# Optimization experiments

Measured on AMD Instinct MI355X. Metric: run time of the kernel, lower is better.

The kernel has to match this reference:

```python
import jax, jax.numpy as jnp
import numpy as np

N_NODES = 100000
N_EDGES = 1600000
IN_FEATS = 256
HEADS = 4
OUT_FEATS = 32


def setup_inputs() -> dict:
    key = jax.random.key(0)
    k1, k2, k3, k4, k5, k6 = jax.random.split(key, 6)
    feat = jax.random.normal(k1, (N_NODES, IN_FEATS), dtype=jnp.float32)
    fc_w = jax.random.normal(k2, (HEADS * OUT_FEATS, IN_FEATS), dtype=jnp.float32) * (1.0 / np.sqrt(IN_FEATS))
    attn_l = jax.random.normal(k3, (1, HEADS, OUT_FEATS), dtype=jnp.float32) * 0.1
    attn_r = jax.random.normal(k4, (1, HEADS, OUT_FEATS), dtype=jnp.float32) * 0.1
    src = jax.random.randint(k5, (N_EDGES,), 0, N_NODES, dtype=jnp.int32)
    dst = jax.random.randint(k6, (N_EDGES,), 0, N_NODES, dtype=jnp.int32)
    return {"feat": feat, "fc_w": fc_w, "attn_l": attn_l, "attn_r": attn_r, "src": src, "dst": dst}


def reference(feat, fc_w, attn_l, attn_r, src, dst):
    # feat: [N, F_in]; fc_w: [H*D, F_in]; attn_l/r: [1, H, D]; src/dst: [E]
    N = feat.shape[0]
    H, D = attn_l.shape[1], attn_l.shape[2]
    # linear projection (no bias), viewed as [N, H, D]
    ft = (feat @ fc_w.T).reshape(N, H, D)
    # per-node attention logits
    el = jnp.einsum('nhd,hd->nh', ft, attn_l[0])  # [N, H]
    er = jnp.einsum('nhd,hd->nh', ft, attn_r[0])  # [N, H]
    # per-edge score: leaky_relu(el[src] + er[dst])
    e = jax.nn.leaky_relu(el[src] + er[dst], negative_slope=0.2)  # [E, H]
    # edge softmax over incoming edges of each dst node (stable)
    emax = jax.ops.segment_max(e, dst, num_segments=N)  # [N, H]
    a = jnp.exp(e - emax[dst])  # [E, H]
    asum = jax.ops.segment_sum(a, dst, num_segments=N)  # [N, H]
    a = a / asum[dst]
    # attn_drop is a no-op in eval mode; weighted scatter-sum aggregation
    msg = ft[src] * a[:, :, None]  # [E, H, D]
    out = jax.ops.segment_sum(msg, dst, num_segments=N)  # [N, H, D]
    # final_layer=False, activation=None, norm=None -> flatten heads
    return out.reshape(N, H * D)
```

## Files before the change

kernel.cpp:

```cpp
#include <hip/hip_runtime.h>
#include <hip/hip_bf16.h>
#include <float.h>

#define IN_F 256
#define HD   128
#define NH   4
#define GM   128

typedef __bf16 bf16x8 __attribute__((ext_vector_type(8)));
typedef __bf16 bf16x2 __attribute__((ext_vector_type(2)));
typedef float  f32x4  __attribute__((ext_vector_type(4)));

__device__ __forceinline__ bf16x8 cvt8(const float4 a, const float4 b) {
    bf16x8 r;
    r[0] = (__bf16)a.x; r[1] = (__bf16)a.y; r[2] = (__bf16)a.z; r[3] = (__bf16)a.w;
    r[4] = (__bf16)b.x; r[5] = (__bf16)b.y; r[6] = (__bf16)b.z; r[7] = (__bf16)b.w;
    return r;
}

__global__ __launch_bounds__(256) void gemm_fused(const float* __restrict__ feat,
                                                  const float* __restrict__ w,
                                                  const float* __restrict__ attn_l,
                                                  const float* __restrict__ attn_r,
                                                  const int* __restrict__ dst,
                                                  __bf16* __restrict__ ft,
                                                  float* __restrict__ el,
                                                  float* __restrict__ er,
                                                  int* __restrict__ deg,
                                                  int* __restrict__ rank,
                                                  int N, int E, int ntiles) {
    __shared__ __align__(16) __bf16 Bs[128][264];
    __shared__ __align__(16) __bf16 As[GM][40];
    const int t = threadIdx.x;
    const int wv = t >> 6;
    const int lane = t & 63;

    {
        const int col = t >> 1;
        const int koff = (t & 1) * 128;
        const float* wp = w + (size_t)col * IN_F + koff;
#pragma unroll
        for (int i = 0; i < 128; i += 8) {
            const float4 v0 = *(const float4*)(wp + i);
            const float4 v1 = *(const float4*)(wp + i + 4);
            *(bf16x8*)&Bs[col][koff + i] = cvt8(v0, v1);
        }
    }

    for (int i = blockIdx.x * 256 + t; i < E; i += gridDim.x * 256)
        rank[i] = atomicAdd(&deg[dst[i]], 1);

    const int frow = lane & 15;
    const int fk   = (lane >> 4) * 8;

    float alw[8], arw[8];
#pragma unroll
    for (int ct = 0; ct < 8; ++ct) {
        alw[ct] = attn_l[ct * 16 + frow];
        arw[ct] = attn_r[ct * 16 + frow];
    }

    const int ar_ = t >> 1;
    const int ac  = (t & 1) * 16;

    float4 p0, p1, p2, p3;
    {
        const int gr = blockIdx.x * GM + ar_;
        if (gr < N) {
            const float* fp = feat + (size_t)gr * IN_F + ac;
            p0 = *(const float4*)(fp);
            p1 = *(const float4*)(fp + 4);
            p2 = *(const float4*)(fp + 8);
            p3 = *(const float4*)(fp + 12);
        } else {
            p0 = p1 = p2 = p3 = make_float4(0.f, 0.f, 0.f, 0.f);
        }
    }

    for (int tile = blockIdx.x; tile < ntiles; tile += gridDim.x) {
        const int row0 = tile * GM;
        f32x4 acc[2][8];
#pragma unroll
        for (int mt = 0; mt < 2; ++mt)
#pragma unroll
            for (int ct = 0; ct < 8; ++ct) acc[mt][ct] = {0.f, 0.f, 0.f, 0.f};

        for (int ks = 0; ks < 8; ++ks) {
            __syncthreads();
            *(bf16x8*)&As[ar_][ac]     = cvt8(p0, p1);
            *(bf16x8*)&As[ar_][ac + 8] = cvt8(p2, p3);

            const int ntile = (ks < 7) ? tile : tile + gridDim.x;
            const int nks   = (ks < 7) ? ks + 1 : 0;
            if (ntile < ntiles) {
                const int gr = ntile * GM + ar_;
                if (gr < N) {
                    const float* fp = feat + (size_t)gr * IN_F + nks * 32 + ac;
                    p0 = *(const float4*)(fp);
                    p1 = *(const float4*)(fp + 4);
                    p2 = *(const float4*)(fp + 8);
                    p3 = *(const float4*)(fp + 12);
                } else {
                    p0 = p1 = p2 = p3 = make_float4(0.f, 0.f, 0.f, 0.f);
                }
            }

            __syncthreads();
            const int k0 = ks * 32;
            const bf16x8 af0 = *(const bf16x8*)&As[wv * 32 + frow][fk];
            const bf16x8 af1 = *(const bf16x8*)&As[wv * 32 + 16 + frow][fk];
#pragma unroll
            for (int ct = 0; ct < 8; ++ct) {
                const bf16x8 bfrag = *(const bf16x8*)&Bs[ct * 16 + frow][k0 + fk];
                acc[0][ct] = __builtin_amdgcn_mfma_f32_16x16x32_bf16(af0, bfrag, acc[0][ct], 0, 0, 0);
                acc[1][ct] = __builtin_amdgcn_mfma_f32_16x16x32_bf16(af1, bfrag, acc[1][ct], 0, 0, 0);
            }
        }

        const int rb = row0 + wv * 32 + (lane >> 4) * 4;
        if (row0 + GM <= N) {
#pragma unroll
            for (int mt = 0; mt < 2; ++mt)
#pragma unroll
                for (int ct = 0; ct < 8; ++ct)
#pragma unroll
                    for (int reg = 0; reg < 4; ++reg) {
                        const int m = rb + mt * 16 + reg;
                        ft[(size_t)m * HD + ct * 16 + frow] = (__bf16)acc[mt][ct][reg];
                    }
        } else {
#pragma unroll
            for (int mt = 0; mt < 2; ++mt)
#pragma unroll
                for (int ct = 0; ct < 8; ++ct)
#pragma unroll
                    for (int reg = 0; reg < 4; ++reg) {
                        const int m = rb + mt * 16 + reg;
                        if (m < N) ft[(size_t)m * HD + ct * 16 + frow] = (__bf16)acc[mt][ct][reg];
                    }
        }

#pragma unroll
        for (int mt = 0; mt < 2; ++mt) {
#pragma unroll
            for (int reg = 0; reg < 4; ++reg) {
                float pl[4], pr[4];
#pragma unroll
                for (int h = 0; h < 4; ++h) {
                    const float v0 = acc[mt][2 * h][reg];
                    const float v1 = acc[mt][2 * h + 1][reg];
                    pl[h] = v0 * alw[2 * h] + v1 * alw[2 * h + 1];
                    pr[h] = v0 * arw[2 * h] + v1 * arw[2 * h + 1];
                }
#pragma unroll
                for (int s = 1; s < 16; s <<= 1) {
#pragma unroll
                    for (int h = 0; h < 4; ++h) {
                        pl[h] += __shfl_xor(pl[h], s);
                        pr[h] += __shfl_xor(pr[h], s);
                    }
                }
                if (frow == 0) {
                    const int r = row0 + wv * 32 + mt * 16 + (lane >> 4) * 4 + reg;
                    if (r < N) {
                        *(float4*)(el + (size_t)r * NH) = make_float4(pl[0], pl[1], pl[2], pl[3]);
                        *(float4*)(er + (size_t)r * NH) = make_float4(pr[0], pr[1], pr[2], pr[3]);
                    }
                }
            }
        }
    }
}

__global__ __launch_bounds__(1024) void scan1_k(const int* __restrict__ deg,
                                                int* __restrict__ off,
                                                int* __restrict__ bsum, int N) {
    __shared__ int lds[1024];
    const int t = threadIdx.x;
    const int g = blockIdx.x * 1024 + t;
    const int x = (g < N) ? deg[g] : 0;
    lds[t] = x;
    __syncthreads();
    int v = x;
    for (int s = 1; s < 1024; s <<= 1) {
        const int add = (t >= s) ? lds[t - s] : 0;
        __syncthreads();
        v += add;
        lds[t] = v;
        __syncthreads();
    }
    if (g < N) off[g] = v - x;
    if (t == 1023) bsum[blockIdx.x] = v;
}

__global__ __launch_bounds__(128) void scan2_k(const int* __restrict__ bsum,
                                               int* __restrict__ boff, int nb) {
    __shared__ int lds[128];
    const int t = threadIdx.x;
    const int x = (t < nb) ? bsum[t] : 0;
    lds[t] = x;
    __syncthreads();
    int v = x;
    for (int s = 1; s < 128; s <<= 1) {
        const int add = (t >= s) ? lds[t - s] : 0;
        __syncthreads();
        v += add;
        lds[t] = v;
        __syncthreads();
    }
    boff[t] = v - x;
}

__global__ __launch_bounds__(256) void scatter_k(const int* __restrict__ src,
                                                 const int* __restrict__ dst,
                                                 const int* __restrict__ off,
                                                 const int* __restrict__ boff,
                                                 const int* __restrict__ rank,
                                                 int* __restrict__ ssrc, int E) {
    const int i = blockIdx.x * 256 + threadIdx.x;
    if (i < E) {
        const int d = dst[i];
        const int p = off[d] + boff[d >> 10] + rank[i];
        ssrc[p] = src[i];
    }
}

__global__ __launch_bounds__(64) void aggregate_k(const __bf16* __restrict__ ft,
                                                  const float* __restrict__ el,
                                                  const float* __restrict__ er,
                                                  const int* __restrict__ deg,
                                                  const int* __restrict__ off,
                                                  const int* __restrict__ boff,
                                                  const int* __restrict__ ssrc,
                                                  float* __restrict__ out, int N) {
    const int n = blockIdx.x;
    const int lane = threadIdx.x;
    const int il = lane & 15;
    const int q  = lane >> 4;
    const int h  = il >> 2;
    float4* outp = (float4*)(out + (size_t)n * HD);
    const int dn = deg[n];
    if (dn == 0) {
        if (q < 2) outp[il * 2 + q] = make_float4(0.f, 0.f, 0.f, 0.f);
        return;
    }
    const int start = off[n] + boff[n >> 10];
    const float4 er4 = *(const float4*)(er + (size_t)n * NH);

    __shared__ float a_lds[64 * NH];
    __shared__ int   s_lds[64];
    float4 ssum = make_float4(0.f, 0.f, 0.f, 0.f);
    float acc[8];
#pragma unroll
    for (int i = 0; i < 8; ++i) acc[i] = 0.f;

    for (int c0 = 0; c0 < dn; c0 += 64) {
        const int j = c0 + lane;
        float4 a = make_float4(0.f, 0.f, 0.f, 0.f);
        int sv = 0;
        if (j < dn) {
            sv = ssrc[start + j];
            float4 e = *(const float4*)(el + (size_t)sv * NH);
            e.x += er4.x; e.y += er4.y; e.z += er4.z; e.w += er4.w;
            e.x = e.x >= 0.f ? e.x : 0.2f * e.x;
            e.y = e.y >= 0.f ? e.y : 0.2f * e.y;
            e.z = e.z >= 0.f ? e.z : 0.2f * e.z;
            e.w = e.w >= 0.f ? e.w : 0.2f * e.w;
            a.x = __expf(e.x); a.y = __expf(e.y);
            a.z = __expf(e.z); a.w = __expf(e.w);
            ssum.x += a.x; ssum.y += a.y; ssum.z += a.z; ssum.w += a.w;
        }
        s_lds[lane] = sv;
        *(float4*)(a_lds + lane * NH) = a;
        __syncthreads();
        const int cnt = min(64, dn - c0);
        for (int j2 = 0; j2 < cnt; j2 += 8) {
            const int e0 = j2 + q;
            const int e1 = j2 + 4 + q;
            const int sv0 = s_lds[e0];
            const int sv1 = s_lds[e1];
            const float a0 = a_lds[e0 * NH + h];
            const float a1 = a_lds[e1 * NH + h];
            const bf16x8 f0 = *(const bf16x8*)(ft + (size_t)sv0 * HD + il * 8);
            const bf16x8 f1 = *(const bf16x8*)(ft + (size_t)sv1 * HD + il * 8);
#pragma unroll
            for (int k = 0; k < 8; ++k) acc[k] = fmaf(a0, (float)f0[k], acc[k]);
#pragma unroll
            for (int k = 0; k < 8; ++k) acc[k] = fmaf(a1, (float)f1[k], acc[k]);
        }
        __syncthreads();
    }
#pragma unroll
    for (int s = 1; s < 64; s <<= 1) {
        ssum.x += __shfl_xor(ssum.x, s);
        ssum.y += __shfl_xor(ssum.y, s);
        ssum.z += __shfl_xor(ssum.z, s);
        ssum.w += __shfl_xor(ssum.w, s);
    }
#pragma unroll
    for (int k = 0; k < 8; ++k) {
        acc[k] += __shfl_xor(acc[k], 16);
        acc[k] += __shfl_xor(acc[k], 32);
    }
    const float sumh = (h == 0) ? ssum.x : (h == 1) ? ssum.y : (h == 2) ? ssum.z : ssum.w;
    const float inv = 1.f / sumh;
    if (q < 2) {
        const int b = q * 4;
        outp[il * 2 + q] = make_float4(acc[b] * inv, acc[b + 1] * inv,
                                       acc[b + 2] * inv, acc[b + 3] * inv);
    }
}

extern "C" void kernel_launch(void* const* d_in, const int* in_sizes, int n_in,
                              void* d_out, int out_size, void* d_ws, size_t ws_size,
                              hipStream_t stream) {
    const float* feat   = (const float*)d_in[0];
    const float* fc_w   = (const float*)d_in[1];
    const float* attn_l = (const float*)d_in[2];
    const float* attn_r = (const float*)d_in[3];
    const int*   src    = (const int*)d_in[4];
    const int*   dst    = (const int*)d_in[5];
    const int N = in_sizes[0] / IN_F;
    const int E = in_sizes[4];
    float* out = (float*)d_out;

    char* wp = (char*)d_ws;
    __bf16* ft = (__bf16*)wp; wp += (size_t)N * HD * 2;
    float* el  = (float*)wp; wp += (size_t)N * NH * 4;
    float* er  = (float*)wp; wp += (size_t)N * NH * 4;
    int* deg   = (int*)wp;   wp += (size_t)N * 4;
    int* off   = (int*)wp;   wp += (size_t)N * 4;
    int* bsum  = (int*)wp;   wp += 1024;
    int* boff  = (int*)wp;   wp += 1024;
    int* rank  = (int*)wp;   wp += (size_t)E * 4;
    int* ssrc  = (int*)wp;   wp += (size_t)E * 4;

    hipMemsetAsync(deg, 0, (size_t)N * 4, stream);

    const int ntiles = (N + GM - 1) / GM;
    gemm_fused<<<dim3(512), dim3(256), 0, stream>>>(feat, fc_w, attn_l, attn_r, dst,
                                                    ft, el, er, deg, rank, N, E, ntiles);
    const int nblk = (N + 1023) >> 10;
    scan1_k<<<dim3(nblk), dim3(1024), 0, stream>>>(deg, off, bsum, N);
    scan2_k<<<dim3(1), dim3(128), 0, stream>>>(bsum, boff, nblk);
    scatter_k<<<dim3((E + 255) / 256), dim3(256), 0, stream>>>(src, dst, off, boff, rank, ssrc, E);
    aggregate_k<<<dim3(N), dim3(64), 0, stream>>>(ft, el, er, deg, off, boff, ssrc, out, N);
}
```

Baseline: 364.6 us.

## Pre-pack weights into MFMA fragment layout and drop LDS staging in GEMM

A new one-block kernel converts fc_w to bf16 once, laid out in MFMA fragment order. The GEMM kernel then reads B fragments straight from global memory (served from cache) and A fragments straight from feat in registers, with no shared memory and no barriers. It also moves from a persistent 512-block grid to one block per 128-row tile. This removes the per-block weight conversion, the LDS traffic and the syncthreads. The cost is an extra kernel launch, uncoalesced 32-byte row reads of feat, and no software prefetch to hide latency.

```diff
diff --git a/kernel.cpp b/kernel.cpp
--- a/kernel.cpp
+++ b/kernel.cpp
@@ -18,8 +18,26 @@
     return r;
 }
 
+__global__ __launch_bounds__(256) void wprep_k(const float* __restrict__ w,
+                                               __bf16* __restrict__ wfrag) {
+    const int t = threadIdx.x;
+    const int col = t >> 1;
+    const int k0 = (t & 1) * 128;
+    const int ct = col >> 4;
+    const float* wp = w + (size_t)col * IN_F + k0;
+#pragma unroll
+    for (int kk = 0; kk < 128; kk += 8) {
+        const float4 v0 = *(const float4*)(wp + kk);
+        const float4 v1 = *(const float4*)(wp + kk + 4);
+        const int k = k0 + kk;
+        const int ks = k >> 5;
+        const int lane = (col & 15) + (((k >> 3) & 3) << 4);
+        *(bf16x8*)(wfrag + ((size_t)(ks * 8 + ct) * 64 + lane) * 8) = cvt8(v0, v1);
+    }
+}
+
 __global__ __launch_bounds__(256) void gemm_fused(const float* __restrict__ feat,
-                                                  const float* __restrict__ w,
+                                                  const __bf16* __restrict__ wfrag,
                                                   const float* __restrict__ attn_l,
                                                   const float* __restrict__ attn_r,
                                                   const int* __restrict__ dst,
@@ -28,30 +46,16 @@
                                                   float* __restrict__ er,
                                                   int* __restrict__ deg,
                                                   int* __restrict__ rank,
-                                                  int N, int E, int ntiles) {
-    __shared__ __align__(16) __bf16 Bs[128][264];
-    __shared__ __align__(16) __bf16 As[GM][40];
+                                                  int N, int E) {
     const int t = threadIdx.x;
+
+    for (int i = blockIdx.x * 256 + t; i < E; i += gridDim.x * 256)
+        rank[i] = atomicAdd(&deg[dst[i]], 1);
+
     const int wv = t >> 6;
     const int lane = t & 63;
-
-    {
-        const int col = t >> 1;
-        const int koff = (t & 1) * 128;
-        const float* wp = w + (size_t)col * IN_F + koff;
-#pragma unroll
-        for (int i = 0; i < 128; i += 8) {
-            const float4 v0 = *(const float4*)(wp + i);
-            const float4 v1 = *(const float4*)(wp + i + 4);
-            *(bf16x8*)&Bs[col][koff + i] = cvt8(v0, v1);
-        }
-    }
-
-    for (int i = blockIdx.x * 256 + t; i < E; i += gridDim.x * 256)
-        rank[i] = atomicAdd(&deg[dst[i]], 1);
-
     const int frow = lane & 15;
-    const int fk   = (lane >> 4) * 8;
+    const int fq   = lane >> 4;
 
     float alw[8], arw[8];
 #pragma unroll
@@ -60,112 +64,96 @@
         arw[ct] = attn_r[ct * 16 + frow];
     }
 
-    const int ar_ = t >> 1;
-    const int ac  = (t & 1) * 16;
-
-    float4 p0, p1, p2, p3;
-    {
-        const int gr = blockIdx.x * GM + ar_;
-        if (gr < N) {
-            const float* fp = feat + (size_t)gr * IN_F + ac;
-            p0 = *(const float4*)(fp);
-            p1 = *(const float4*)(fp + 4);
-            p2 = *(const float4*)(fp + 8);
-            p3 = *(const float4*)(fp + 12);
+    const int row0 = blockIdx.x * GM;
+    const int r0 = row0 + wv * 32 + frow;
+    const int r1 = r0 + 16;
+    const bool ok0 = r0 < N;
+    const bool ok1 = r1 < N;
+    const float* fA0 = feat + (size_t)r0 * IN_F + fq * 8;
+    const float* fA1 = feat + (size_t)r1 * IN_F + fq * 8;
+    const __bf16* wfl = wfrag + (size_t)lane * 8;
+
+    f32x4 acc[2][8];
+#pragma unroll
+    for (int mt = 0; mt < 2; ++mt)
+#pragma unroll
+        for (int ct = 0; ct < 8; ++ct) acc[mt][ct] = {0.f, 0.f, 0.f, 0.f};
+
+#pragma unroll
+    for (int ks = 0; ks < 8; ++ks) {
+        bf16x8 af0, af1;
+        if (ok0) {
+            const float4 a = *(const float4*)(fA0 + ks * 32);
+            const float4 b = *(const float4*)(fA0 + ks * 32 + 4);
+            af0 = cvt8(a, b);
         } else {
-            p0 = p1 = p2 = p3 = make_float4(0.f, 0.f, 0.f, 0.f);
-        }
-    }
-
-    for (int tile = blockIdx.x; tile < ntiles; tile += gridDim.x) {
-        const int row0 = tile * GM;
-        f32x4 acc[2][8];
+#pragma unroll
+            for (int i = 0; i < 8; ++i) af0[i] = (__bf16)0.f;
+        }
+        if (ok1) {
+            const float4 a = *(const float4*)(fA1 + ks * 32);
+            const float4 b = *(const float4*)(fA1 + ks * 32 + 4);
+            af1 = cvt8(a, b);
+        } else {
+#pragma unroll
+            for (int i = 0; i < 8; ++i) af1[i] = (__bf16)0.f;
+        }
+#pragma unroll
+        for (int ct = 0; ct < 8; ++ct) {
+            const bf16x8 bfrag = *(const bf16x8*)(wfl + (size_t)(ks * 8 + ct) * 512);
+            acc[0][ct] = __builtin_amdgcn_mfma_f32_16x16x32_bf16(af0, bfrag, acc[0][ct], 0, 0, 0);
+            acc[1][ct] = __builtin_amdgcn_mfma_f32_16x16x32_bf16(af1, bfrag, acc[1][ct], 0, 0, 0);
+        }
+    }
+
+    const int rb = row0 + wv * 32 + (lane >> 4) * 4;
+    if (row0 + GM <= N) {
 #pragma unroll
         for (int mt = 0; mt < 2; ++mt)
 #pragma unroll
-            for (int ct = 0; ct < 8; ++ct) acc[mt][ct] = {0.f, 0.f, 0.f, 0.f};
-
-        for (int ks = 0; ks < 8; ++ks) {
-            __syncthreads();
-            *(bf16x8*)&As[ar_][ac]     = cvt8(p0, p1);
-            *(bf16x8*)&As[ar_][ac + 8] = cvt8(p2, p3);
-
-            const int ntile = (ks < 7) ? tile : tile + gridDim.x;
-            const int nks   = (ks < 7) ? ks + 1 : 0;
-            if (ntile < ntiles) {
-                const int gr = ntile * GM + ar_;
-                if (gr < N) {
-                    const float* fp = feat + (size_t)gr * IN_F + nks * 32 + ac;
-                    p0 = *(const float4*)(fp);
-                    p1 = *(const float4*)(fp + 4);
-                    p2 = *(const float4*)(fp + 8);
-                    p3 = *(const float4*)(fp + 12);
-                } else {
-                    p0 = p1 = p2 = p3 = make_float4(0.f, 0.f, 0.f, 0.f);
+            for (int ct = 0; ct < 8; ++ct)
+#pragma unroll
+                for (int reg = 0; reg < 4; ++reg) {
+                    const int m = rb + mt * 16 + reg;
+                    ft[(size_t)m * HD + ct * 16 + frow] = (__bf16)acc[mt][ct][reg];
+                }
+    } else {
+#pragma unroll
+        for (int mt = 0; mt < 2; ++mt)
+#pragma unroll
+            for (int ct = 0; ct < 8; ++ct)
+#pragma unroll
+                for (int reg = 0; reg < 4; ++reg) {
+                    const int m = rb + mt * 16 + reg;
+                    if (m < N) ft[(size_t)m * HD + ct * 16 + frow] = (__bf16)acc[mt][ct][reg];
+                }
+    }
+
+#pragma unroll
+    for (int mt = 0; mt < 2; ++mt) {
+#pragma unroll
+        for (int reg = 0; reg < 4; ++reg) {
+            float pl[4], pr[4];
+#pragma unroll
+            for (int h = 0; h < 4; ++h) {
+                const float v0 = acc[mt][2 * h][reg];
+                const float v1 = acc[mt][2 * h + 1][reg];
+                pl[h] = v0 * alw[2 * h] + v1 * alw[2 * h + 1];
+                pr[h] = v0 * arw[2 * h] + v1 * arw[2 * h + 1];
+            }
+#pragma unroll
+            for (int s = 1; s < 16; s <<= 1) {
+#pragma unroll
+                for (int h = 0; h < 4; ++h) {
+                    pl[h] += __shfl_xor(pl[h], s);
+                    pr[h] += __shfl_xor(pr[h], s);
                 }
             }
-
-            __syncthreads();
-            const int k0 = ks * 32;
-            const bf16x8 af0 = *(const bf16x8*)&As[wv * 32 + frow][fk];
-            const bf16x8 af1 = *(const bf16x8*)&As[wv * 32 + 16 + frow][fk];
-#pragma unroll
-            for (int ct = 0; ct < 8; ++ct) {
-                const bf16x8 bfrag = *(const bf16x8*)&Bs[ct * 16 + frow][k0 + fk];
-                acc[0][ct] = __builtin_amdgcn_mfma_f32_16x16x32_bf16(af0, bfrag, acc[0][ct], 0, 0, 0);
-                acc[1][ct] = __builtin_amdgcn_mfma_f32_16x16x32_bf16(af1, bfrag, acc[1][ct], 0, 0, 0);
-            }
-        }
-
-        const int rb = row0 + wv * 32 + (lane >> 4) * 4;
-        if (row0 + GM <= N) {
-#pragma unroll
-            for (int mt = 0; mt < 2; ++mt)
-#pragma unroll
-                for (int ct = 0; ct < 8; ++ct)
-#pragma unroll
-                    for (int reg = 0; reg < 4; ++reg) {
-                        const int m = rb + mt * 16 + reg;
-                        ft[(size_t)m * HD + ct * 16 + frow] = (__bf16)acc[mt][ct][reg];
-                    }
-        } else {
-#pragma unroll
-            for (int mt = 0; mt < 2; ++mt)
-#pragma unroll
-                for (int ct = 0; ct < 8; ++ct)
-#pragma unroll
-                    for (int reg = 0; reg < 4; ++reg) {
-                        const int m = rb + mt * 16 + reg;
-                        if (m < N) ft[(size_t)m * HD + ct * 16 + frow] = (__bf16)acc[mt][ct][reg];
-                    }
-        }
-
-#pragma unroll
-        for (int mt = 0; mt < 2; ++mt) {
-#pragma unroll
-            for (int reg = 0; reg < 4; ++reg) {
-                float pl[4], pr[4];
-#pragma unroll
-                for (int h = 0; h < 4; ++h) {
-                    const float v0 = acc[mt][2 * h][reg];
-                    const float v1 = acc[mt][2 * h + 1][reg];
-                    pl[h] = v0 * alw[2 * h] + v1 * alw[2 * h + 1];
-                    pr[h] = v0 * arw[2 * h] + v1 * arw[2 * h + 1];
-                }
-#pragma unroll
-                for (int s = 1; s < 16; s <<= 1) {
-#pragma unroll
-                    for (int h = 0; h < 4; ++h) {
-                        pl[h] += __shfl_xor(pl[h], s);
-                        pr[h] += __shfl_xor(pr[h], s);
-                    }
-                }
-                if (frow == 0) {
-                    const int r = row0 + wv * 32 + mt * 16 + (lane >> 4) * 4 + reg;
-                    if (r < N) {
-                        *(float4*)(el + (size_t)r * NH) = make_float4(pl[0], pl[1], pl[2], pl[3]);
-                        *(float4*)(er + (size_t)r * NH) = make_float4(pr[0], pr[1], pr[2], pr[3]);
-                    }
+            if (frow == 0) {
+                const int r = row0 + wv * 32 + mt * 16 + (lane >> 4) * 4 + reg;
+                if (r < N) {
+                    *(float4*)(el + (size_t)r * NH) = make_float4(pl[0], pl[1], pl[2], pl[3]);
+                    *(float4*)(er + (size_t)r * NH) = make_float4(pr[0], pr[1], pr[2], pr[3]);
                 }
             }
         }
@@ -334,12 +322,14 @@
     int* boff  = (int*)wp;   wp += 1024;
     int* rank  = (int*)wp;   wp += (size_t)E * 4;
     int* ssrc  = (int*)wp;   wp += (size_t)E * 4;
+    __bf16* wfrag = (__bf16*)wp; wp += (size_t)HD * IN_F * 2;
 
     hipMemsetAsync(deg, 0, (size_t)N * 4, stream);
 
     const int ntiles = (N + GM - 1) / GM;
-    gemm_fused<<<dim3(512), dim3(256), 0, stream>>>(feat, fc_w, attn_l, attn_r, dst,
-                                                    ft, el, er, deg, rank, N, E, ntiles);
+    wprep_k<<<dim3(1), dim3(256), 0, stream>>>(fc_w, wfrag);
+    gemm_fused<<<dim3(ntiles), dim3(256), 0, stream>>>(feat, wfrag, attn_l, attn_r, dst,
+                                                       ft, el, er, deg, rank, N, E);
     const int nblk = (N + 1023) >> 10;
     scan1_k<<<dim3(nblk), dim3(1024), 0, stream>>>(deg, off, bsum, N);
     scan2_k<<<dim3(1), dim3(128), 0, stream>>>(bsum, boff, nblk);
```

New measurement: 390.6 us. +7.1%, slower.
